# Optimization experiments

Hardware: AMD Instinct MI355X
Metric: run time of the kernel (lower is better)

## Reference

```python
import jax, jax.numpy as jnp
import numpy as np

B, NT, K = 2048, 8192, 128   # traces, time samples, spline knots
DT = 1e-3


def setup_inputs() -> dict:
    key = jax.random.key(0)
    k1, k2, k3 = jax.random.split(key, 3)
    t = jnp.arange(NT, dtype=jnp.float32) * DT                       # uniform grid
    f = jax.random.uniform(k1, (B, NT), dtype=jnp.float32) + 0.1     # positive densities
    # normalize each trace to unit trapezoid mass so the CDF F lies in [0, 1]
    mass = (0.5 * (f[:, :1] + f[:, -1:]) + f[:, 1:-1].sum(-1, keepdims=True)) * DT
    f = f / mass
    # per-trace monotone knot grids on [0, 1] (spline breakpoints of the quantile fn)
    interior = jnp.sort(jax.random.uniform(k2, (B, K - 2), dtype=jnp.float32), axis=-1)
    knots = jnp.concatenate(
        [jnp.zeros((B, 1), jnp.float32), interior, jnp.full((B, 1), 1.0 + 1e-6, jnp.float32)],
        axis=-1,
    )
    # piecewise-cubic coefficients (a, b, c, d) per interval
    coeffs = 0.1 * jax.random.normal(k3, (B, K - 1, 4), dtype=jnp.float32)
    return {"f": f, "t": t, "knots": knots, "coeffs": coeffs}


def _cum_trap(f, dt):
    # cumulative trapezoid along last dim, zero-prepended (preserve_dims=True)
    inc = 0.5 * (f[..., 1:] + f[..., :-1]) * dt
    u = jnp.cumsum(inc, axis=-1)
    zero = jnp.zeros(u.shape[:-1] + (1,), u.dtype)
    return jnp.concatenate([zero, u], axis=-1)


def _spline_eval(knots, coeffs, q):
    # knots: [K], coeffs: [K-1, 4], q: [nt] -> [nt]
    idx = jnp.clip(jnp.searchsorted(knots, q, side="right") - 1, 0, knots.shape[0] - 2)
    dx = q - knots[idx]
    c = coeffs[idx]  # [nt, 4]
    return c[..., 0] + dx * (c[..., 1] + dx * (c[..., 2] + dx * c[..., 3]))


def reference(f, t, knots, coeffs):
    dt = t[1] - t[0]
    F = _cum_trap(f, dt)                               # [B, NT] CDF
    off_diag = jax.vmap(_spline_eval)(knots, coeffs, F)  # batched spline lookup
    g = (t - off_diag) ** 2 * f                        # broadcast t over batch
    # trapezoid reduction with uniform dx
    return (0.5 * (g[..., 0] + g[..., -1]) + g[..., 1:-1].sum(-1)) * dt
```

## Files before the change

### kernel.cpp

```cpp
#include <hip/hip_runtime.h>


#define NT 8192
#define K 128
#define NTHREADS 512
#define ELEMS (NT / NTHREADS)
#define NWAVES (NTHREADS / 64)
#define LUTG 256

__global__ __launch_bounds__(NTHREADS) void w2loss_kernel(
    const float* __restrict__ f,
    const float* __restrict__ t,
    const float* __restrict__ knots,
    const float* __restrict__ coeffs,
    float* __restrict__ out)
{
    const int b    = blockIdx.x;
    const int tid  = threadIdx.x;
    const int lane = tid & 63;
    const int wave = tid >> 6;

    __shared__ float  s_knots[K];
    __shared__ float4 s_coeffs[K - 1];
    __shared__ int    s_lut[LUTG];
    __shared__ float  s_wsum[NWAVES];
    __shared__ float  s_wred[NWAVES];
    __shared__ float  s_f0;

    if (tid < K) s_knots[tid] = knots[(size_t)b * K + tid];
    if (tid < K - 1)
        s_coeffs[tid] =
            reinterpret_cast<const float4*>(coeffs + (size_t)b * (K - 1) * 4)[tid];

    const float4* fb4 =
        reinterpret_cast<const float4*>(f + (size_t)b * NT + tid * ELEMS);
    float fv[ELEMS];
#pragma unroll
    for (int i = 0; i < ELEMS / 4; ++i) {
        float4 v = fb4[i];
        fv[4 * i + 0] = v.x; fv[4 * i + 1] = v.y;
        fv[4 * i + 2] = v.z; fv[4 * i + 3] = v.w;
    }

    float local = 0.f;
#pragma unroll
    for (int i = 0; i < ELEMS; ++i) local += fv[i];

    float scan = local;
#pragma unroll
    for (int d = 1; d < 64; d <<= 1) {
        float up = __shfl_up(scan, d, 64);
        if (lane >= d) scan += up;
    }
    if (lane == 63) s_wsum[wave] = scan;
    if (tid == 0)  s_f0 = fv[0];
    __syncthreads();

    if (tid < LUTG) {
        float gval = (float)tid * (1.0f / (float)LUTG);
        int p = 0;
#pragma unroll
        for (int step = 64; step >= 1; step >>= 1) {
            int np = p + step;
            if (np <= K - 1 && s_knots[np] <= gval) p = np;
        }
        s_lut[tid] = p;
    }
    __syncthreads();

    float wv = (lane < NWAVES) ? s_wsum[lane] : 0.f;
#pragma unroll
    for (int d = 1; d < NWAVES; d <<= 1) {
        float up = __shfl_up(wv, d, 64);
        if (lane >= d) wv += up;
    }
    const float waveoff = (wave == 0) ? 0.f : __shfl(wv, wave - 1, 64);

    const float f0      = s_f0;
    const float dt      = t[1] - t[0];
    const float half_dt = 0.5f * dt;

    const float S_incl_first = waveoff + (scan - local) + fv[0];
    float F = (S_incl_first - 0.5f * (f0 + fv[0])) * dt;

    const int   base = tid * ELEMS;
    const float tb   = (float)base * dt;

    int g  = (int)(F * (float)LUTG);
    g      = g > (LUTG - 1) ? (LUTG - 1) : (g < 0 ? 0 : g);
    int i0 = s_lut[g];
    while (i0 < K - 2 && s_knots[i0 + 1] <= F) ++i0;
    float  kn0_lo = s_knots[i0];
    float  kn0_hi = s_knots[i0 + 1];
    float4 c0     = s_coeffs[i0];
    int    j1     = (i0 < K - 2) ? i0 + 1 : K - 2;
    float4 c1     = s_coeffs[j1];
    float  kn1_hi = (i0 + 2 <= K - 1) ? s_knots[i0 + 2] : 3.4e38f;

    float acc, term_first, term_last = 0.f;
    {
        float dx = F - kn0_lo;
        float sp = c0.x + dx * (c0.y + dx * (c0.z + dx * c0.w));
        float d0 = tb - sp;
        term_first = d0 * d0 * fv[0];
        acc = term_first;
    }

#pragma unroll
    for (int i = 1; i < ELEMS; ++i) {
        F = fmaf(fv[i - 1] + fv[i], half_dt, F);

        if (kn1_hi <= F) {
            int idx = i0 + 2;
            while (idx < K - 2 && s_knots[idx + 1] <= F) ++idx;
            i0     = idx;
            kn0_lo = s_knots[i0];
            kn0_hi = s_knots[i0 + 1];
            c0     = s_coeffs[i0];
            j1     = (i0 < K - 2) ? i0 + 1 : K - 2;
            c1     = s_coeffs[j1];
            kn1_hi = (i0 + 2 <= K - 1) ? s_knots[i0 + 2] : 3.4e38f;
        }

        bool  use1 = (kn0_hi <= F);
        float klo  = use1 ? kn0_hi : kn0_lo;
        float cx   = use1 ? c1.x : c0.x;
        float cy   = use1 ? c1.y : c0.y;
        float cz   = use1 ? c1.z : c0.z;
        float cw   = use1 ? c1.w : c0.w;

        float dx = F - klo;
        float sp = cx + dx * (cy + dx * (cz + dx * cw));
        float tt = fmaf((float)i, dt, tb);
        float d  = tt - sp;
        float term = d * d * fv[i];
        acc += term;
        if (i == ELEMS - 1) term_last = term;
    }

    if (base == 0)          acc -= 0.5f * term_first;
    if (base + ELEMS == NT) acc -= 0.5f * term_last;

#pragma unroll
    for (int d = 32; d >= 1; d >>= 1) acc += __shfl_down(acc, d, 64);
    if (lane == 0) s_wred[wave] = acc;
    __syncthreads();
    if (tid == 0) {
        float r = 0.f;
#pragma unroll
        for (int w = 0; w < NWAVES; ++w) r += s_wred[w];
        out[b] = r * dt;
    }
}

extern "C" void kernel_launch(void* const* d_in, const int* in_sizes, int n_in,
                              void* d_out, int out_size, void* d_ws, size_t ws_size,
                              hipStream_t stream) {
    const float* f      = (const float*)d_in[0];
    const float* t      = (const float*)d_in[1];
    const float* knots  = (const float*)d_in[2];
    const float* coeffs = (const float*)d_in[3];
    float* out          = (float*)d_out;

    const int Btr = in_sizes[0] / NT;
    w2loss_kernel<<<Btr, NTHREADS, 0, stream>>>(f, t, knots, coeffs, out);
}
```

Baseline: 121.8 us.

## Map one trace per wavefront with chunked scan and register prefetch

Restructures the kernel so each 64-lane wavefront processes a whole trace in 8 sequential chunks of 1024 samples. It keeps a running carry across chunks in place of the block-wide scan and cross-wave reduction, and prefetches the next chunk's data into registers while the current one is computed. This removes the block-level synchronization and shared-memory scan, at the cost of serial chunk processing per trace and fewer resident waves per trace. Grid size drops to traces/4 blocks, which assumes the trace count is divisible by 4.

```diff
diff --git a/kernel.cpp b/kernel.cpp
--- a/kernel.cpp
+++ b/kernel.cpp
@@ -3,9 +3,11 @@
 
 #define NT 8192
 #define K 128
-#define NTHREADS 512
-#define ELEMS (NT / NTHREADS)
-#define NWAVES (NTHREADS / 64)
+#define NTHREADS 256
+#define WPB (NTHREADS / 64)
+#define PER_LANE 16
+#define CHUNK (64 * PER_LANE)
+#define NCHUNK (NT / CHUNK)
 #define LUTG 256
 
 __global__ __launch_bounds__(NTHREADS) void w2loss_kernel(
@@ -15,142 +17,136 @@
     const float* __restrict__ coeffs,
     float* __restrict__ out)
 {
-    const int b    = blockIdx.x;
-    const int tid  = threadIdx.x;
-    const int lane = tid & 63;
-    const int wave = tid >> 6;
+    const int tid   = threadIdx.x;
+    const int ln    = tid & 63;
+    const int w     = tid >> 6;
+    const int trace = blockIdx.x * WPB + w;
 
-    __shared__ float  s_knots[K];
-    __shared__ float4 s_coeffs[K - 1];
-    __shared__ int    s_lut[LUTG];
-    __shared__ float  s_wsum[NWAVES];
-    __shared__ float  s_wred[NWAVES];
-    __shared__ float  s_f0;
+    __shared__ float  s_knots[WPB][K];
+    __shared__ float4 s_coeffs[WPB][K - 1];
+    __shared__ int    s_lut[WPB][LUTG];
 
-    if (tid < K) s_knots[tid] = knots[(size_t)b * K + tid];
-    if (tid < K - 1)
-        s_coeffs[tid] =
-            reinterpret_cast<const float4*>(coeffs + (size_t)b * (K - 1) * 4)[tid];
-
-    const float4* fb4 =
-        reinterpret_cast<const float4*>(f + (size_t)b * NT + tid * ELEMS);
-    float fv[ELEMS];
-#pragma unroll
-    for (int i = 0; i < ELEMS / 4; ++i) {
-        float4 v = fb4[i];
-        fv[4 * i + 0] = v.x; fv[4 * i + 1] = v.y;
-        fv[4 * i + 2] = v.z; fv[4 * i + 3] = v.w;
-    }
-
-    float local = 0.f;
-#pragma unroll
-    for (int i = 0; i < ELEMS; ++i) local += fv[i];
-
-    float scan = local;
-#pragma unroll
-    for (int d = 1; d < 64; d <<= 1) {
-        float up = __shfl_up(scan, d, 64);
-        if (lane >= d) scan += up;
-    }
-    if (lane == 63) s_wsum[wave] = scan;
-    if (tid == 0)  s_f0 = fv[0];
+    for (int j = ln; j < K; j += 64)
+        s_knots[w][j] = knots[(size_t)trace * K + j];
+    const float4* cf =
+        reinterpret_cast<const float4*>(coeffs + (size_t)trace * (K - 1) * 4);
+    for (int j = ln; j < K - 1; j += 64)
+        s_coeffs[w][j] = cf[j];
     __syncthreads();
 
-    if (tid < LUTG) {
-        float gval = (float)tid * (1.0f / (float)LUTG);
-        int p = 0;
+#pragma unroll
+    for (int q = 0; q < LUTG / 64; ++q) {
+        int   cell = q * 64 + ln;
+        float gval = (float)cell * (1.0f / (float)LUTG);
+        int   p    = 0;
 #pragma unroll
         for (int step = 64; step >= 1; step >>= 1) {
             int np = p + step;
-            if (np <= K - 1 && s_knots[np] <= gval) p = np;
+            if (np <= K - 1 && s_knots[w][np] <= gval) p = np;
         }
-        s_lut[tid] = p;
+        s_lut[w][cell] = p;
     }
     __syncthreads();
 
-    float wv = (lane < NWAVES) ? s_wsum[lane] : 0.f;
+    const float  dt = t[1] - t[0];
+    const float* fb = f + (size_t)trace * NT;
+
+    float4 a0, a1, a2, a3;
+    {
+        const float4* p4 = reinterpret_cast<const float4*>(fb) + ln * (PER_LANE / 4);
+        a0 = p4[0]; a1 = p4[1]; a2 = p4[2]; a3 = p4[3];
+    }
+    const float f0 = __shfl(a0.x, 0, 64);
+
+    float carry = 0.f, acc = 0.f, term_first = 0.f, term_last = 0.f;
+
+    for (int c = 0; c < NCHUNK; ++c) {
+        float4 b0, b1, b2, b3;
+        if (c + 1 < NCHUNK) {
+            const float4* p4 =
+                reinterpret_cast<const float4*>(fb + (c + 1) * CHUNK) + ln * (PER_LANE / 4);
+            b0 = p4[0]; b1 = p4[1]; b2 = p4[2]; b3 = p4[3];
+        } else {
+            b0 = a0; b1 = a1; b2 = a2; b3 = a3;
+        }
+
+        float fv[PER_LANE];
+        fv[0]=a0.x; fv[1]=a0.y; fv[2]=a0.z; fv[3]=a0.w;
+        fv[4]=a1.x; fv[5]=a1.y; fv[6]=a1.z; fv[7]=a1.w;
+        fv[8]=a2.x; fv[9]=a2.y; fv[10]=a2.z; fv[11]=a2.w;
+        fv[12]=a3.x; fv[13]=a3.y; fv[14]=a3.z; fv[15]=a3.w;
+
+        float psum = 0.f;
 #pragma unroll
-    for (int d = 1; d < NWAVES; d <<= 1) {
-        float up = __shfl_up(wv, d, 64);
-        if (lane >= d) wv += up;
-    }
-    const float waveoff = (wave == 0) ? 0.f : __shfl(wv, wave - 1, 64);
+        for (int k = 0; k < PER_LANE; ++k) psum += fv[k];
 
-    const float f0      = s_f0;
-    const float dt      = t[1] - t[0];
-    const float half_dt = 0.5f * dt;
+        float scan = psum;
+#pragma unroll
+        for (int d = 1; d < 64; d <<= 1) {
+            float up = __shfl_up(scan, d, 64);
+            if (ln >= d) scan += up;
+        }
+        const float excl = carry + (scan - psum);
+        carry += __shfl(scan, 63, 64);
 
-    const float S_incl_first = waveoff + (scan - local) + fv[0];
-    float F = (S_incl_first - 0.5f * (f0 + fv[0])) * dt;
+        float Ffirst = (excl + fv[0] - 0.5f * (f0 + fv[0])) * dt;
+        int g  = (int)(Ffirst * (float)LUTG);
+        g      = g > (LUTG - 1) ? (LUTG - 1) : (g < 0 ? 0 : g);
+        int i0 = s_lut[w][g];
+        while (i0 < K - 2 && s_knots[w][i0 + 1] <= Ffirst) ++i0;
+        float  kn0_lo = s_knots[w][i0];
+        float  kn0_hi = s_knots[w][i0 + 1];
+        float4 c0     = s_coeffs[w][i0];
+        int    j1     = (i0 < K - 2) ? i0 + 1 : K - 2;
+        float4 c1     = s_coeffs[w][j1];
+        float  kn1_hi = (i0 + 2 <= K - 1) ? s_knots[w][i0 + 2] : 3.4e38f;
 
-    const int   base = tid * ELEMS;
-    const float tb   = (float)base * dt;
+        const float tbase = (float)(c * CHUNK + ln * PER_LANE) * dt;
+        float s = 0.f;
 
-    int g  = (int)(F * (float)LUTG);
-    g      = g > (LUTG - 1) ? (LUTG - 1) : (g < 0 ? 0 : g);
-    int i0 = s_lut[g];
-    while (i0 < K - 2 && s_knots[i0 + 1] <= F) ++i0;
-    float  kn0_lo = s_knots[i0];
-    float  kn0_hi = s_knots[i0 + 1];
-    float4 c0     = s_coeffs[i0];
-    int    j1     = (i0 < K - 2) ? i0 + 1 : K - 2;
-    float4 c1     = s_coeffs[j1];
-    float  kn1_hi = (i0 + 2 <= K - 1) ? s_knots[i0 + 2] : 3.4e38f;
+#pragma unroll
+        for (int k = 0; k < PER_LANE; ++k) {
+            s += fv[k];
+            float F = (excl + s - 0.5f * (f0 + fv[k])) * dt;
 
-    float acc, term_first, term_last = 0.f;
-    {
-        float dx = F - kn0_lo;
-        float sp = c0.x + dx * (c0.y + dx * (c0.z + dx * c0.w));
-        float d0 = tb - sp;
-        term_first = d0 * d0 * fv[0];
-        acc = term_first;
+            if (kn1_hi <= F) {
+                int idx = i0 + 2;
+                while (idx < K - 2 && s_knots[w][idx + 1] <= F) ++idx;
+                i0     = idx > K - 2 ? K - 2 : idx;
+                kn0_lo = s_knots[w][i0];
+                kn0_hi = s_knots[w][i0 + 1];
+                c0     = s_coeffs[w][i0];
+                j1     = (i0 < K - 2) ? i0 + 1 : K - 2;
+                c1     = s_coeffs[w][j1];
+                kn1_hi = (i0 + 2 <= K - 1) ? s_knots[w][i0 + 2] : 3.4e38f;
+            }
+
+            bool  use1 = (kn0_hi <= F);
+            float klo  = use1 ? kn0_hi : kn0_lo;
+            float cx   = use1 ? c1.x : c0.x;
+            float cy   = use1 ? c1.y : c0.y;
+            float cz   = use1 ? c1.z : c0.z;
+            float cw   = use1 ? c1.w : c0.w;
+
+            float dx = F - klo;
+            float sp = cx + dx * (cy + dx * (cz + dx * cw));
+            float tt = fmaf((float)k, dt, tbase);
+            float d  = tt - sp;
+            float term = d * d * fv[k];
+            acc += term;
+            if (k == 0 && c == 0)                     term_first = term;
+            if (k == PER_LANE - 1 && c == NCHUNK - 1) term_last  = term;
+        }
+
+        a0 = b0; a1 = b1; a2 = b2; a3 = b3;
     }
 
-#pragma unroll
-    for (int i = 1; i < ELEMS; ++i) {
-        F = fmaf(fv[i - 1] + fv[i], half_dt, F);
-
-        if (kn1_hi <= F) {
-            int idx = i0 + 2;
-            while (idx < K - 2 && s_knots[idx + 1] <= F) ++idx;
-            i0     = idx;
-            kn0_lo = s_knots[i0];
-            kn0_hi = s_knots[i0 + 1];
-            c0     = s_coeffs[i0];
-            j1     = (i0 < K - 2) ? i0 + 1 : K - 2;
-            c1     = s_coeffs[j1];
-            kn1_hi = (i0 + 2 <= K - 1) ? s_knots[i0 + 2] : 3.4e38f;
-        }
-
-        bool  use1 = (kn0_hi <= F);
-        float klo  = use1 ? kn0_hi : kn0_lo;
-        float cx   = use1 ? c1.x : c0.x;
-        float cy   = use1 ? c1.y : c0.y;
-        float cz   = use1 ? c1.z : c0.z;
-        float cw   = use1 ? c1.w : c0.w;
-
-        float dx = F - klo;
-        float sp = cx + dx * (cy + dx * (cz + dx * cw));
-        float tt = fmaf((float)i, dt, tb);
-        float d  = tt - sp;
-        float term = d * d * fv[i];
-        acc += term;
-        if (i == ELEMS - 1) term_last = term;
-    }
-
-    if (base == 0)          acc -= 0.5f * term_first;
-    if (base + ELEMS == NT) acc -= 0.5f * term_last;
+    if (ln == 0)  acc -= 0.5f * term_first;
+    if (ln == 63) acc -= 0.5f * term_last;
 
 #pragma unroll
     for (int d = 32; d >= 1; d >>= 1) acc += __shfl_down(acc, d, 64);
-    if (lane == 0) s_wred[wave] = acc;
-    __syncthreads();
-    if (tid == 0) {
-        float r = 0.f;
-#pragma unroll
-        for (int w = 0; w < NWAVES; ++w) r += s_wred[w];
-        out[b] = r * dt;
-    }
+    if (ln == 0) out[trace] = acc * dt;
 }
 
 extern "C" void kernel_launch(void* const* d_in, const int* in_sizes, int n_in,
@@ -162,6 +158,7 @@
     const float* coeffs = (const float*)d_in[3];
     float* out          = (float*)d_out;
 
-    const int Btr = in_sizes[0] / NT;
-    w2loss_kernel<<<Btr, NTHREADS, 0, stream>>>(f, t, knots, coeffs, out);
+    const int traces = in_sizes[0] / NT;
+    const int blocks = traces / WPB;
+    w2loss_kernel<<<blocks, NTHREADS, 0, stream>>>(f, t, knots, coeffs, out);
 }
```

New measurement: 105.5 us. 1.15x faster.
